# Kernel optimization log

Measured on AMD Instinct MI355X. Metric: run time of the kernel, lower is better.

## Reference

```python
import jax, jax.numpy as jnp
import numpy as np

D_MODEL = 192
NODE_NUM = 64
DEPTH = 2
ALPHA = 0.05
NUM_LAYERS = 2
LN_EPS = 1e-5


def _gcn(x, p):
    # x: [N, in_dim*D_MODEL]; faithful port of GCN.forward (eval mode)
    nv1, nv2, ws, bs, wm, bm, we, be, wl, bl, g, b = p
    N = x.shape[0]
    in_dim = x.shape[1] // D_MODEL
    adp = jax.nn.softmax(jax.nn.relu(nv1 @ nv2), axis=1)            # [V,V]
    adj = adp + jnp.eye(NODE_NUM, dtype=x.dtype)
    a = adj / adj.sum(1, keepdims=True)                              # row-normalized
    h0 = jax.lax.conv_general_dilated(
        x.reshape(N, in_dim, D_MODEL), ws, (1,), 'VALID',
        dimension_numbers=('NCH', 'OIH', 'NCH')) + bs[None, :, None]  # [N,C,V]
    h = h0
    outs = [h0]
    for _ in range(DEPTH):
        h = ALPHA * h0 + (1.0 - ALPHA) * jnp.einsum('ncw,vw->ncv', h, a)
        outs.append(h)
    ho = jnp.concatenate(outs, axis=1)                               # [N,(DEPTH+1)C,V]
    ho = jax.nn.gelu(jnp.einsum('ncv,oc->nov', ho, wm) + bm[None, :, None], approximate=False)
    ho = jnp.einsum('ncv,oc->nov', ho, we) + be[None, :, None]       # [N,6,V]
    ho = jnp.einsum('nov,dv->nod', ho, wl) + bl                      # [N,6,D]
    mu = ho.mean(-1, keepdims=True)
    var = ((ho - mu) ** 2).mean(-1, keepdims=True)                   # biased, like torch LN
    ho = (ho - mu) / jnp.sqrt(var + LN_EPS) * g + b
    return ho.reshape(N, 6 * D_MODEL)


def _encoder(inp4, flag, layer_params):
    x = jnp.transpose(inp4, (2, 0, 1, 3)) if flag == 1 else jnp.transpose(inp4, (1, 0, 2, 3))
    W, B, O, D = x.shape
    L = W + O - 1
    N = W * B
    # input_transfer: shift row r by r along the slice axis
    place = jax.vmap(lambda xr, r: jax.lax.dynamic_update_slice(
        jnp.zeros((B, L, D), x.dtype), xr, (0, r, 0)))
    a = place(x, jnp.arange(W)).reshape(N, L, D)
    layer0_output = None
    output_all = None
    rows_layers, cols_layers = [], []
    for layer in range(NUM_LAYERS):
        if layer >= 1:
            a = output_all  # eval mode: F.dropout is identity
            if layer == 1:
                layer0_output = a
        p = layer_params[layer]

        def step(carry, x_t, p=p):
            h_row, h_col = carry
            gate = _gcn(jnp.concatenate([h_row, h_col, x_t], axis=-1), p)  # [N,6D]
            sg = jax.nn.sigmoid(gate[:, :4 * D])
            tg = jnp.tanh(gate[:, 4 * D:])
            ug_r, og_r, ug_c, og_c = jnp.split(sg, 4, axis=-1)
            ig_r, ig_c = jnp.split(tg, 2, axis=-1)
            h_row = jnp.tanh((1.0 - ug_r) * h_row + ug_r * ig_r) * og_r
            h_col = jnp.tanh((1.0 - ug_c) * h_col + ug_c * ig_c) * og_c
            out_s = jnp.concatenate([h_row, h_col], axis=-1)
            # col hidden is saved pre-roll, rolled for next step
            return (h_row, jnp.roll(h_col, B, axis=0)), (out_s, h_row, h_col)

        init = (jnp.zeros((N, D), x.dtype), jnp.zeros((N, D), x.dtype))
        _, (outs, hrows, hcols) = jax.lax.scan(step, init, jnp.swapaxes(a, 0, 1))
        output_all = jnp.swapaxes(outs, 0, 1)                        # [N,L,2D]
        if layer >= 1:
            output_all = output_all + layer0_output
        # rows saved at slice s>=O-1 from block loc = s-O+1
        rows = hrows.reshape(L, W, B, D)[jnp.arange(O - 1, L), jnp.arange(W)]  # [W,B,D]
        # cols saved at slice s>=W-1 from last batch block
        cols = hcols[W - 1:, (W - 1) * B:, :]                        # [O,B,D]
        rows_layers.append(rows)
        cols_layers.append(cols)
    hidden_row_all = jnp.stack(rows_layers).transpose(2, 0, 1, 3)    # [B,layers,W,D]
    hidden_col_all = jnp.stack(cols_layers).transpose(2, 0, 1, 3)    # [B,layers,O,D]
    if flag == 1:
        return output_all, hidden_col_all, hidden_row_all
    return output_all, hidden_row_all, hidden_col_all


def setup_inputs() -> dict:
    key = jax.random.key(0)
    ks = jax.random.split(key, 20)
    idx = [0]
    def nxt():
        k = ks[idx[0]]
        idx[0] += 1
        return k
    B, W, O = 8, 24, 48
    K = D_MODEL - NODE_NUM + 1  # 129
    cc, sc, nd = 16, 32, 40
    d = {"input": jax.random.normal(nxt(), (B, W, O, D_MODEL), dtype=jnp.float32)}
    for li, in_dim in enumerate([3, 4]):
        d[f"nodevec1_{li}"] = jax.random.normal(nxt(), (NODE_NUM, nd), dtype=jnp.float32)
        d[f"nodevec2_{li}"] = jax.random.normal(nxt(), (nd, NODE_NUM), dtype=jnp.float32)
        d[f"w_start_{li}"] = jax.random.normal(nxt(), (cc, in_dim, K), dtype=jnp.float32) * 0.05
        d[f"b_start_{li}"] = jnp.zeros((cc,), jnp.float32)
        d[f"w_mlp_{li}"] = jax.random.normal(nxt(), (sc, (DEPTH + 1) * cc), dtype=jnp.float32) * 0.05
        d[f"b_mlp_{li}"] = jnp.zeros((sc,), jnp.float32)
        d[f"w_end_{li}"] = jax.random.normal(nxt(), (6, sc), dtype=jnp.float32) * 0.05
        d[f"b_end_{li}"] = jnp.zeros((6,), jnp.float32)
        d[f"w_lin_{li}"] = jax.random.normal(nxt(), (D_MODEL, NODE_NUM), dtype=jnp.float32) * 0.05
        d[f"b_lin_{li}"] = jnp.zeros((D_MODEL,), jnp.float32)
        d[f"gamma_{li}"] = jnp.ones((D_MODEL,), jnp.float32)
        d[f"beta_{li}"] = jnp.zeros((D_MODEL,), jnp.float32)
    d["flag"] = 0
    return d


def reference(input, nodevec1_0, nodevec2_0, w_start_0, b_start_0, w_mlp_0, b_mlp_0,
              w_end_0, b_end_0, w_lin_0, b_lin_0, gamma_0, beta_0,
              nodevec1_1, nodevec2_1, w_start_1, b_start_1, w_mlp_1, b_mlp_1,
              w_end_1, b_end_1, w_lin_1, b_lin_1, gamma_1, beta_1, flag):
    p0 = (nodevec1_0, nodevec2_0, w_start_0, b_start_0, w_mlp_0, b_mlp_0,
          w_end_0, b_end_0, w_lin_0, b_lin_0, gamma_0, beta_0)
    p1 = (nodevec1_1, nodevec2_1, w_start_1, b_start_1, w_mlp_1, b_mlp_1,
          w_end_1, b_end_1, w_lin_1, b_lin_1, gamma_1, beta_1)
    return _encoder(input, flag, (p0, p1))
```

## Files before the change

### kernel.cpp

```cpp
#include <hip/hip_runtime.h>
#include <hip/hip_bf16.h>

#define NT 512
typedef unsigned short u16;
typedef unsigned long long u64;

__device__ __forceinline__ u16 tobf(float x) {
  union { __hip_bfloat16 h; u16 u; } cv;
  cv.h = __float2bfloat16(x);
  return cv.u;
}
__device__ __forceinline__ float frombf(u16 u) {
  return __uint_as_float(((unsigned)u) << 16);
}
__device__ __forceinline__ float sigf(float x) {
  return __builtin_amdgcn_rcpf(1.f + __builtin_amdgcn_exp2f(-1.4426950408889634f * x));
}
__device__ __forceinline__ float tanh_fast(float x) {
  return 1.f - 2.f * __builtin_amdgcn_rcpf(1.f + __builtin_amdgcn_exp2f(2.8853900817779268f * x));
}
__device__ __forceinline__ void lds_fence() {
  asm volatile("s_waitcnt lgkmcnt(0)" ::: "memory");
  __builtin_amdgcn_sched_barrier(0);
}
__device__ __forceinline__ void bar_light() {
  asm volatile("s_waitcnt lgkmcnt(0)" ::: "memory");
  __builtin_amdgcn_s_barrier();
  asm volatile("" ::: "memory");
}

struct SeqArgs {
  const float* input;
  const float* nv1_0; const float* nv2_0; const float* nv1_1; const float* nv2_1;
  const float* w_start0; const float* b_start0; const float* w_mlp0; const float* b_mlp0;
  const float* w_end0;   const float* b_end0;   const float* w_lin0; const float* b_lin0;
  const float* gamma0;   const float* beta0;
  const float* w_start1; const float* b_start1; const float* w_mlp1; const float* b_mlp1;
  const float* w_end1;   const float* b_end1;   const float* w_lin1; const float* b_lin1;
  const float* gamma1;   const float* beta1;
  u64*   HCOL2;
  int*   prog;
  float* out_all; float* out_hrow; float* out_hcol;
};

__global__ __launch_bounds__(NT, 2) void seq_kernel(SeqArgs A) {
  const int n = blockIdx.x, w = n >> 3, b = n & 7, tid = threadIdx.x;
  const int pred = (n + 184) % 192;
  const int succ = (n + 8) % 192;

  __shared__ __align__(16) float sCIN[768];
  __shared__ __align__(16) u16   sWS[64 * 132];
  __shared__ __align__(16) float sAT[4096];
  __shared__ __align__(16) float sH[2][1024];
  __shared__ __align__(16) float sAbuf[4928];
  float* const sPart = sAbuf;
  float* const sG    = sAbuf;
  float* const sH2c  = sAbuf + 2048;
  float* const sE    = sAbuf + 2048;
  float* const sY    = sAbuf;
  float* const smWE  = sAbuf + 3072;
  float* const smBE  = sAbuf + 3264;
  float* const smWM  = sAbuf + 3328;

  for (int layer = 0; layer < 2; ++layer) {
    const int in_dim = 3 + layer;
    const int P = in_dim - 1;
    const float* nv1    = layer ? A.nv1_1    : A.nv1_0;
    const float* nv2    = layer ? A.nv2_1    : A.nv2_0;
    const float* wstart = layer ? A.w_start1 : A.w_start0;
    const float* bs     = layer ? A.b_start1 : A.b_start0;
    const float* wm     = layer ? A.w_mlp1   : A.w_mlp0;
    const float* bm     = layer ? A.b_mlp1   : A.b_mlp0;
    const float* we     = layer ? A.w_end1   : A.w_end0;
    const float* be     = layer ? A.b_end1   : A.b_end0;
    const float* wl     = layer ? A.w_lin1   : A.w_lin0;
    const float* bl     = layer ? A.b_lin1   : A.b_lin0;
    const float* gm     = layer ? A.gamma1   : A.gamma0;
    const float* bt     = layer ? A.beta1    : A.beta0;

    for (int idx = tid; idx < 4096; idx += NT) {
      int v = idx >> 6, ww = idx & 63;
      float s = 0.f;
      for (int j = 0; j < 40; ++j) s = fmaf(nv1[v*40 + j], nv2[j*64 + ww], s);
      sAbuf[idx] = fmaxf(s, 0.f);
    }
    __syncthreads();
    if (tid < 64) {
      const int v = tid;
      float m = -1e30f;
      for (int ww = 0; ww < 64; ++ww) m = fmaxf(m, sAbuf[v*64 + ww]);
      float s = 0.f;
      for (int ww = 0; ww < 64; ++ww) { float e = expf(sAbuf[v*64 + ww] - m); sAbuf[v*64 + ww] = e; s += e; }
      float inv = 1.f / s, rs = 1.f;
      for (int ww = 0; ww < 64; ++ww) rs += sAbuf[v*64 + ww] * inv;
      float irs = 1.f / rs;
      for (int ww = 0; ww < 64; ++ww) {
        float a = sAbuf[v*64 + ww] * inv + ((ww == v) ? 1.f : 0.f);
        sAT[ww*64 + v] = a * irs;
      }
    }
    __syncthreads();
    for (int idx = tid; idx < 16*in_dim*132; idx += NT) {
      int row = idx / 132, k = idx - row*132;
      sWS[idx] = (k < 129) ? tobf(wstart[((row & 15)*in_dim + (row >> 4))*129 + k]) : (u16)0;
    }
    for (int idx = tid; idx < 1536; idx += NT) { int o = idx/48, c = idx - o*48; smWM[o*50 + c] = wm[idx]; }
    for (int idx = tid; idx < 192; idx += NT) smWE[idx] = we[idx];
    if (tid < 6) smBE[tid] = be[tid];
    for (int d = tid; d < 384; d += NT) sCIN[d] = 0.f;

    const int v_p = tid & 63;
    const int o0  = tid >> 6;
    const float bmv0 = bm[o0], bmv1 = bm[o0 + 8], bmv2 = bm[o0 + 16], bmv3 = bm[o0 + 24];
    float blv = 0.f, gmv = 1.f, btv = 0.f;
    if (tid < 384) blv = bl[(tid >= 192) ? tid - 192 : tid];
    if (tid < 192) { gmv = gm[tid]; btv = bt[tid]; }
    float bs_r[2];
    bs_r[0] = bs[tid >> 6];
    bs_r[1] = bs[(tid >> 6) + 8];
    __syncthreads();

    auto pre_conv = [&]() {
      const int nslots = P << 8;
      for (int s = tid; s < nslots; s += NT) {
        const int cidx = s >> 4;
        const int p = cidx >> 4, c = cidx & 15;
        const int vg = s & 15;
        const int ich = (p == 0) ? 0 : (p + 1);
        const float* xin = ((p == 0) ? &sCIN[0] : &sCIN[384 + (p-1)*192]) + vg*4;
        const u16* wrow = &sWS[(ich*16 + c)*132];
        float a0 = 0.f, a1 = 0.f, a2 = 0.f, a3 = 0.f;
        float4 xc = *(const float4*)xin;
        for (int k4 = 0; k4 < 128; k4 += 4) {
          ushort4 wu = *(const ushort4*)(wrow + k4);
          float w0 = frombf(wu.x), w1 = frombf(wu.y), w2 = frombf(wu.z), w3 = frombf(wu.w);
          float4 xn = *(const float4*)(xin + k4 + 4);
          a0 = fmaf(w3, xc.w, fmaf(w2, xc.z, fmaf(w1, xc.y, fmaf(w0, xc.x, a0))));
          a1 = fmaf(w3, xn.x, fmaf(w2, xc.w, fmaf(w1, xc.z, fmaf(w0, xc.y, a1))));
          a2 = fmaf(w3, xn.y, fmaf(w2, xn.x, fmaf(w1, xc.w, fmaf(w0, xc.z, a2))));
          a3 = fmaf(w3, xn.z, fmaf(w2, xn.y, fmaf(w1, xn.x, fmaf(w0, xc.w, a3))));
          xc = xn;
        }
        float wk = frombf(wrow[128]);
        a0 = fmaf(wk, xc.x, a0); a1 = fmaf(wk, xc.y, a1);
        a2 = fmaf(wk, xc.z, a2); a3 = fmaf(wk, xc.w, a3);
        *(float4*)&sPart[cidx*64 + vg*4] = make_float4(a0, a1, a2, a3);
      }
      bar_light();
      {
        const int c0 = tid >> 6, v = tid & 63;
        float sum0 = bs_r[0], sum1 = bs_r[1];
        for (int p = 0; p < P; ++p) {
          sum0 += sPart[(p*16 + c0     )*64 + v];
          sum1 += sPart[(p*16 + c0 + 8 )*64 + v];
        }
        sH[0][ c0      *64 + v] = sum0;
        sH[0][(c0 + 8 )*64 + v] = sum1;
      }
      bar_light();
    };

    {
      if (layer == 0) {
        int o = 0 - w;
        if (o >= 0 && o < 48) {
          const float* xr = A.input + (((size_t)(b*24 + w)*48 + o)*192);
          for (int d = tid; d < 192; d += NT) sCIN[384 + d] = xr[d];
        } else {
          for (int d = tid; d < 192; d += NT) sCIN[384 + d] = 0.f;
        }
      } else {
        const float* xr = A.out_all + ((size_t)n*71 + 0)*384;
        for (int d = tid; d < 384; d += NT) sCIN[384 + d] = xr[d];
      }
      bar_light();
      pre_conv();
    }

    for (int t = 0; t < 71; ++t) {
      const int S = layer*71 + t;

      float xpa = 0.f, xpb = 0.f;
      if (t < 70 && tid < 192) {
        if (layer == 0) {
          int o = (t + 1) - w;
          if (o >= 0 && o < 48)
            xpa = A.input[(((size_t)(b*24 + w)*48 + o)*192) + tid];
        } else {
          const float* xr = A.out_all + ((size_t)n*71 + (t+1))*384;
          xpa = xr[tid];
          xpb = xr[192 + tid];
        }
      }

      if (t > 0) {
        if (tid < 192) {
          const u64* src = &A.HCOL2[((size_t)((S-1) & 15)*192 + pred)*192 + tid];
          u64 v;
          do {
            v = __hip_atomic_load(src, __ATOMIC_RELAXED, __HIP_MEMORY_SCOPE_AGENT);
          } while ((unsigned)(v >> 32) != (unsigned)S);
          sCIN[192 + tid] = __uint_as_float((unsigned)v);
        } else if (tid == 256 && S >= 16) {
          while (__hip_atomic_load(&A.prog[succ*32], __ATOMIC_RELAXED, __HIP_MEMORY_SCOPE_AGENT) < S - 15)
            __builtin_amdgcn_s_sleep(2);
        }
        bar_light();
        if (tid == 0)
          __hip_atomic_store(&A.prog[n*32], S, __ATOMIC_RELAXED, __HIP_MEMORY_SCOPE_AGENT);
      } else if (S >= 16) {
        if (tid == 256) {
          while (__hip_atomic_load(&A.prog[succ*32], __ATOMIC_RELAXED, __HIP_MEMORY_SCOPE_AGENT) < S - 15)
            __builtin_amdgcn_s_sleep(2);
        }
      }

      {
        const int c = tid >> 5, vg2 = tid & 31;
        const int vbase = c*64 + vg2*2;
        const float* xin = &sCIN[192 + vg2*2];
        const u16* wrow = &sWS[(16 + c)*132];
        float a0 = sH[0][vbase], a1 = sH[0][vbase + 1];
        float2 xc = *(const float2*)xin;
        for (int k2 = 0; k2 < 128; k2 += 2) {
          ushort2 wu = *(const ushort2*)(wrow + k2);
          float w0 = frombf(wu.x), w1 = frombf(wu.y);
          float2 xn = *(const float2*)(xin + k2 + 2);
          a0 = fmaf(w1, xc.y, fmaf(w0, xc.x, a0));
          a1 = fmaf(w1, xn.x, fmaf(w0, xc.y, a1));
          xc = xn;
        }
        float wk = frombf(wrow[128]);
        a0 = fmaf(wk, xc.x, a0); a1 = fmaf(wk, xc.y, a1);
        sH[0][vbase] = a0; sH[0][vbase + 1] = a1;
      }
      lds_fence();
      {
        const int c0 = o0 * 2;
        float pa0 = 0.f, pa1 = 0.f;
        for (int w4 = 0; w4 < 64; w4 += 4) {
          float a0v = sAT[(w4+0)*64 + v_p];
          float a1v = sAT[(w4+1)*64 + v_p];
          float a2v = sAT[(w4+2)*64 + v_p];
          float a3v = sAT[(w4+3)*64 + v_p];
          float4 h0v = *(const float4*)&sH[0][ c0      *64 + w4];
          float4 h1v = *(const float4*)&sH[0][(c0 + 1 )*64 + w4];
          pa0 = fmaf(h0v.x, a0v, pa0); pa0 = fmaf(h0v.y, a1v, pa0);
          pa0 = fmaf(h0v.z, a2v, pa0); pa0 = fmaf(h0v.w, a3v, pa0);
          pa1 = fmaf(h1v.x, a0v, pa1); pa1 = fmaf(h1v.y, a1v, pa1);
          pa1 = fmaf(h1v.z, a2v, pa1); pa1 = fmaf(h1v.w, a3v, pa1);
        }
        float h0a = sH[0][ c0      *64 + v_p];
        float h0b = sH[0][(c0 + 1 )*64 + v_p];
        sH[1][ c0      *64 + v_p] = fmaf(0.95f, pa0, 0.05f * h0a);
        sH[1][(c0 + 1 )*64 + v_p] = fmaf(0.95f, pa1, 0.05f * h0b);
        lds_fence();
        float pb0 = 0.f, pb1 = 0.f;
        for (int w4 = 0; w4 < 64; w4 += 4) {
          float a0v = sAT[(w4+0)*64 + v_p];
          float a1v = sAT[(w4+1)*64 + v_p];
          float a2v = sAT[(w4+2)*64 + v_p];
          float a3v = sAT[(w4+3)*64 + v_p];
          float4 h0v = *(const float4*)&sH[1][ c0      *64 + w4];
          float4 h1v = *(const float4*)&sH[1][(c0 + 1 )*64 + w4];
          pb0 = fmaf(h0v.x, a0v, pb0); pb0 = fmaf(h0v.y, a1v, pb0);
          pb0 = fmaf(h0v.z, a2v, pb0); pb0 = fmaf(h0v.w, a3v, pb0);
          pb1 = fmaf(h1v.x, a0v, pb1); pb1 = fmaf(h1v.y, a1v, pb1);
          pb1 = fmaf(h1v.z, a2v, pb1); pb1 = fmaf(h1v.w, a3v, pb1);
        }
        sH2c[ c0      *64 + v_p] = fmaf(0.95f, pb0, 0.05f * h0a);
        sH2c[(c0 + 1 )*64 + v_p] = fmaf(0.95f, pb1, 0.05f * h0b);
      }
      bar_light();

      {
        float g0 = bmv0, g1 = bmv1, g2 = bmv2, g3 = bmv3;
#pragma unroll
        for (int c = 0; c < 16; ++c) {
          float h0v = sH[0][c*64 + v_p];
          float h1v = sH[1][c*64 + v_p];
          float h2v = sH2c[c*64 + v_p];
          g0 = fmaf(smWM[(o0     )*50 + c], h0v, fmaf(smWM[(o0     )*50 + 16 + c], h1v, fmaf(smWM[(o0     )*50 + 32 + c], h2v, g0)));
          g1 = fmaf(smWM[(o0 +  8)*50 + c], h0v, fmaf(smWM[(o0 +  8)*50 + 16 + c], h1v, fmaf(smWM[(o0 +  8)*50 + 32 + c], h2v, g1)));
          g2 = fmaf(smWM[(o0 + 16)*50 + c], h0v, fmaf(smWM[(o0 + 16)*50 + 16 + c], h1v, fmaf(smWM[(o0 + 16)*50 + 32 + c], h2v, g2)));
          g3 = fmaf(smWM[(o0 + 24)*50 + c], h0v, fmaf(smWM[(o0 + 24)*50 + 16 + c], h1v, fmaf(smWM[(o0 + 24)*50 + 32 + c], h2v, g3)));
        }
        g0 = 0.5f * g0 * (1.f + erff(g0 * 0.70710678118654752f));
        g1 = 0.5f * g1 * (1.f + erff(g1 * 0.70710678118654752f));
        g2 = 0.5f * g2 * (1.f + erff(g2 * 0.70710678118654752f));
        g3 = 0.5f * g3 * (1.f + erff(g3 * 0.70710678118654752f));
        sG[(o0     )*64 + v_p] = g0;
        sG[(o0 +  8)*64 + v_p] = g1;
        sG[(o0 + 16)*64 + v_p] = g2;
        sG[(o0 + 24)*64 + v_p] = g3;
      }
      bar_light();

      for (int idx = tid; idx < 384; idx += NT) {
        int o2 = idx >> 6, v = idx & 63;
        float acc = smBE[o2];
        for (int c = 0; c < 32; ++c) acc = fmaf(smWE[o2*32 + c], sG[c*64 + v], acc);
        sE[idx] = acc;
      }
      bar_light();

      if (tid < 384) {
        const int d  = (tid >= 192) ? tid - 192 : tid;
        const int r0 = (tid >= 192) ? 3 : 0;
        const float4* wrow = (const float4*)(wl + d*64);
        float y0 = blv, y1 = blv, y2 = blv;
        for (int q = 0; q < 16; ++q) {
          float4 wv = wrow[q];
          float4 e0 = *(const float4*)&sE[(r0+0)*64 + q*4];
          float4 e1 = *(const float4*)&sE[(r0+1)*64 + q*4];
          float4 e2 = *(const float4*)&sE[(r0+2)*64 + q*4];
          y0 = fmaf(e0.x,wv.x, fmaf(e0.y,wv.y, fmaf(e0.z,wv.z, fmaf(e0.w,wv.w, y0))));
          y1 = fmaf(e1.x,wv.x, fmaf(e1.y,wv.y, fmaf(e1.z,wv.z, fmaf(e1.w,wv.w, y1))));
          y2 = fmaf(e2.x,wv.x, fmaf(e2.y,wv.y, fmaf(e2.z,wv.z, fmaf(e2.w,wv.w, y2))));
        }
        sY[(r0+0)*192 + d] = y0;
        sY[(r0+1)*192 + d] = y1;
        sY[(r0+2)*192 + d] = y2;
      }
      bar_light();

      if (tid < 192) {
        const int r = tid >> 5, l32 = tid & 31;
        float sm = 0.f, sq = 0.f;
#pragma unroll
        for (int m = 0; m < 6; ++m) {
          float v = sY[r*192 + l32 + 32*m];
          sm += v; sq = fmaf(v, v, sq);
        }
#pragma unroll
        for (int off = 16; off >= 1; off >>= 1) {
          sm += __shfl_xor(sm, off);
          sq += __shfl_xor(sq, off);
        }
        if (l32 == 0) {
          float mu = sm * (1.f/192.f);
          float var = sq * (1.f/192.f) - mu*mu;
          sH[1][r] = mu;
          sH[1][8 + r] = rsqrtf(fmaxf(var, 0.f) + 1e-5f);
        }
      }
      bar_light();

      float hcn = 0.f;
      if (tid < 192) {
        const int d = tid;
        float y2 = fmaf((sY[2*192+d] - sH[1][2]) * sH[1][10], gmv, btv);
        float y3 = fmaf((sY[3*192+d] - sH[1][3]) * sH[1][11], gmv, btv);
        float y5 = fmaf((sY[5*192+d] - sH[1][5]) * sH[1][13], gmv, btv);
        float ugc = sigf(y2), ogc = sigf(y3), igc = tanh_fast(y5);
        float hc = sCIN[192 + d];
        hcn = tanh_fast(fmaf(ugc, igc, (1.f - ugc)*hc)) * ogc;
        u64 pk = ((u64)(unsigned)(S + 1) << 32) | (u64)__float_as_uint(hcn);
        __hip_atomic_store(&A.HCOL2[((size_t)(S & 15)*192 + n)*192 + d], pk,
                           __ATOMIC_RELAXED, __HIP_MEMORY_SCOPE_AGENT);
      }
      if (tid < 192) {
        const int d = tid;
        float y0 = fmaf((sY[0*192+d] - sH[1][0]) * sH[1][8],  gmv, btv);
        float y1 = fmaf((sY[1*192+d] - sH[1][1]) * sH[1][9],  gmv, btv);
        float y4 = fmaf((sY[4*192+d] - sH[1][4]) * sH[1][12], gmv, btv);
        float ugr = sigf(y0), ogr = sigf(y1), igr = tanh_fast(y4);
        float hr = sCIN[d];
        float hrn = tanh_fast(fmaf(ugr, igr, (1.f - ugr)*hr)) * ogr;
        sCIN[d] = hrn;
        float* oa = A.out_all + ((size_t)n*71 + t)*384;
        if (layer == 0) { oa[d] = hrn; oa[192 + d] = hcn; }
        else           { oa[d] = hrn + sCIN[384 + d]; oa[192 + d] = hcn + sCIN[576 + d]; }
        if (t == 47 + w)
          A.out_hrow[(((size_t)b*2 + layer)*24 + w)*192 + d] = hrn;
        if (w == 23 && t >= 23)
          A.out_hcol[(((size_t)b*2 + layer)*48 + (t - 23))*192 + d] = hcn;
        if (t < 70) {
          sCIN[384 + d] = xpa;
          if (layer == 1) sCIN[576 + d] = xpb;
        }
      }
      bar_light();
      if (t < 70) pre_conv();
    }
    __syncthreads();
  }
}

extern "C" void kernel_launch(void* const* d_in, const int* in_sizes, int n_in,
                              void* d_out, int out_size, void* d_ws, size_t ws_size,
                              hipStream_t stream) {
  (void)in_sizes; (void)n_in; (void)out_size; (void)ws_size;
  char* ws = (char*)d_ws;
  int* prog  = (int*)ws;
  u64* HCOL2 = (u64*)(ws + 24576);

  hipMemsetAsync(ws, 0, 24576 + 4718592, stream);

  SeqArgs A;
  A.input    = (const float*)d_in[0];
  A.nv1_0    = (const float*)d_in[1];  A.nv2_0 = (const float*)d_in[2];
  A.w_start0 = (const float*)d_in[3];  A.b_start0 = (const float*)d_in[4];
  A.w_mlp0   = (const float*)d_in[5];  A.b_mlp0   = (const float*)d_in[6];
  A.w_end0   = (const float*)d_in[7];  A.b_end0   = (const float*)d_in[8];
  A.w_lin0   = (const float*)d_in[9];  A.b_lin0   = (const float*)d_in[10];
  A.gamma0   = (const float*)d_in[11]; A.beta0    = (const float*)d_in[12];
  A.nv1_1    = (const float*)d_in[13]; A.nv2_1 = (const float*)d_in[14];
  A.w_start1 = (const float*)d_in[15]; A.b_start1 = (const float*)d_in[16];
  A.w_mlp1   = (const float*)d_in[17]; A.b_mlp1   = (const float*)d_in[18];
  A.w_end1   = (const float*)d_in[19]; A.b_end1   = (const float*)d_in[20];
  A.w_lin1   = (const float*)d_in[21]; A.b_lin1   = (const float*)d_in[22];
  A.gamma1   = (const float*)d_in[23]; A.beta1    = (const float*)d_in[24];
  A.HCOL2 = HCOL2; A.prog = prog;
  A.out_all  = (float*)d_out;
  A.out_hrow = (float*)d_out + 5234688;
  A.out_hcol = (float*)d_out + 5308416;

  seq_kernel<<<192, NT, 0, stream>>>(A);
}
```

Before: 2.644 ms.

## Double block size, split next-input prefetch to spare waves, double-buffer inputs

The block grows to 1024 threads. The first 512 threads run the recurrent conv and graph propagation. The other 512 prefetch the next step's input directly into a double-buffered LDS slot and poll the successor's progress flag. Work in pre_conv and the MLP stage is repartitioned so each thread handles fewer outputs, and the hcol spin-wait now sleeps between polls. This aims to hide global-load latency and shorten per-step critical-path work, at the cost of more waves per block and fewer idle lanes in some phases.

```diff
diff --git a/kernel.cpp b/kernel.cpp
--- a/kernel.cpp
+++ b/kernel.cpp
@@ -1,7 +1,7 @@
 #include <hip/hip_runtime.h>
 #include <hip/hip_bf16.h>
 
-#define NT 512
+#define NT 1024
 typedef unsigned short u16;
 typedef unsigned long long u64;
 
@@ -43,12 +43,12 @@
   float* out_all; float* out_hrow; float* out_hcol;
 };
 
-__global__ __launch_bounds__(NT, 2) void seq_kernel(SeqArgs A) {
+__global__ __launch_bounds__(NT, 4) void seq_kernel(SeqArgs A) {
   const int n = blockIdx.x, w = n >> 3, b = n & 7, tid = threadIdx.x;
   const int pred = (n + 184) % 192;
   const int succ = (n + 8) % 192;
 
-  __shared__ __align__(16) float sCIN[768];
+  __shared__ __align__(16) float sCIN[1152];
   __shared__ __align__(16) u16   sWS[64 * 132];
   __shared__ __align__(16) float sAT[4096];
   __shared__ __align__(16) float sH[2][1024];
@@ -111,116 +111,24 @@
 
     const int v_p = tid & 63;
     const int o0  = tid >> 6;
-    const float bmv0 = bm[o0], bmv1 = bm[o0 + 8], bmv2 = bm[o0 + 16], bmv3 = bm[o0 + 24];
+    const float bmv0 = bm[o0], bmv1 = bm[o0 + 16];
     float blv = 0.f, gmv = 1.f, btv = 0.f;
     if (tid < 384) blv = bl[(tid >= 192) ? tid - 192 : tid];
     if (tid < 192) { gmv = gm[tid]; btv = bt[tid]; }
-    float bs_r[2];
-    bs_r[0] = bs[tid >> 6];
-    bs_r[1] = bs[(tid >> 6) + 8];
+    const float bs_r0 = bs[o0];
     __syncthreads();
 
-    auto pre_conv = [&]() {
-      const int nslots = P << 8;
+    auto pre_conv = [&](int parity) {
+      const float* xb = &sCIN[384 + parity*384];
+      const int nslots = P << 9;
       for (int s = tid; s < nslots; s += NT) {
-        const int cidx = s >> 4;
+        const int cidx = s >> 5;
+        const int vg2  = s & 31;
         const int p = cidx >> 4, c = cidx & 15;
-        const int vg = s & 15;
         const int ich = (p == 0) ? 0 : (p + 1);
-        const float* xin = ((p == 0) ? &sCIN[0] : &sCIN[384 + (p-1)*192]) + vg*4;
+        const float* xin = ((p == 0) ? &sCIN[0] : &xb[(p-1)*192]) + vg2*2;
         const u16* wrow = &sWS[(ich*16 + c)*132];
-        float a0 = 0.f, a1 = 0.f, a2 = 0.f, a3 = 0.f;
-        float4 xc = *(const float4*)xin;
-        for (int k4 = 0; k4 < 128; k4 += 4) {
-          ushort4 wu = *(const ushort4*)(wrow + k4);
-          float w0 = frombf(wu.x), w1 = frombf(wu.y), w2 = frombf(wu.z), w3 = frombf(wu.w);
-          float4 xn = *(const float4*)(xin + k4 + 4);
-          a0 = fmaf(w3, xc.w, fmaf(w2, xc.z, fmaf(w1, xc.y, fmaf(w0, xc.x, a0))));
-          a1 = fmaf(w3, xn.x, fmaf(w2, xc.w, fmaf(w1, xc.z, fmaf(w0, xc.y, a1))));
-          a2 = fmaf(w3, xn.y, fmaf(w2, xn.x, fmaf(w1, xc.w, fmaf(w0, xc.z, a2))));
-          a3 = fmaf(w3, xn.z, fmaf(w2, xn.y, fmaf(w1, xn.x, fmaf(w0, xc.w, a3))));
-          xc = xn;
-        }
-        float wk = frombf(wrow[128]);
-        a0 = fmaf(wk, xc.x, a0); a1 = fmaf(wk, xc.y, a1);
-        a2 = fmaf(wk, xc.z, a2); a3 = fmaf(wk, xc.w, a3);
-        *(float4*)&sPart[cidx*64 + vg*4] = make_float4(a0, a1, a2, a3);
-      }
-      bar_light();
-      {
-        const int c0 = tid >> 6, v = tid & 63;
-        float sum0 = bs_r[0], sum1 = bs_r[1];
-        for (int p = 0; p < P; ++p) {
-          sum0 += sPart[(p*16 + c0     )*64 + v];
-          sum1 += sPart[(p*16 + c0 + 8 )*64 + v];
-        }
-        sH[0][ c0      *64 + v] = sum0;
-        sH[0][(c0 + 8 )*64 + v] = sum1;
-      }
-      bar_light();
-    };
-
-    {
-      if (layer == 0) {
-        int o = 0 - w;
-        if (o >= 0 && o < 48) {
-          const float* xr = A.input + (((size_t)(b*24 + w)*48 + o)*192);
-          for (int d = tid; d < 192; d += NT) sCIN[384 + d] = xr[d];
-        } else {
-          for (int d = tid; d < 192; d += NT) sCIN[384 + d] = 0.f;
-        }
-      } else {
-        const float* xr = A.out_all + ((size_t)n*71 + 0)*384;
-        for (int d = tid; d < 384; d += NT) sCIN[384 + d] = xr[d];
-      }
-      bar_light();
-      pre_conv();
-    }
-
-    for (int t = 0; t < 71; ++t) {
-      const int S = layer*71 + t;
-
-      float xpa = 0.f, xpb = 0.f;
-      if (t < 70 && tid < 192) {
-        if (layer == 0) {
-          int o = (t + 1) - w;
-          if (o >= 0 && o < 48)
-            xpa = A.input[(((size_t)(b*24 + w)*48 + o)*192) + tid];
-        } else {
-          const float* xr = A.out_all + ((size_t)n*71 + (t+1))*384;
-          xpa = xr[tid];
-          xpb = xr[192 + tid];
-        }
-      }
-
-      if (t > 0) {
-        if (tid < 192) {
-          const u64* src = &A.HCOL2[((size_t)((S-1) & 15)*192 + pred)*192 + tid];
-          u64 v;
-          do {
-            v = __hip_atomic_load(src, __ATOMIC_RELAXED, __HIP_MEMORY_SCOPE_AGENT);
-          } while ((unsigned)(v >> 32) != (unsigned)S);
-          sCIN[192 + tid] = __uint_as_float((unsigned)v);
-        } else if (tid == 256 && S >= 16) {
-          while (__hip_atomic_load(&A.prog[succ*32], __ATOMIC_RELAXED, __HIP_MEMORY_SCOPE_AGENT) < S - 15)
-            __builtin_amdgcn_s_sleep(2);
-        }
-        bar_light();
-        if (tid == 0)
-          __hip_atomic_store(&A.prog[n*32], S, __ATOMIC_RELAXED, __HIP_MEMORY_SCOPE_AGENT);
-      } else if (S >= 16) {
-        if (tid == 256) {
-          while (__hip_atomic_load(&A.prog[succ*32], __ATOMIC_RELAXED, __HIP_MEMORY_SCOPE_AGENT) < S - 15)
-            __builtin_amdgcn_s_sleep(2);
-        }
-      }
-
-      {
-        const int c = tid >> 5, vg2 = tid & 31;
-        const int vbase = c*64 + vg2*2;
-        const float* xin = &sCIN[192 + vg2*2];
-        const u16* wrow = &sWS[(16 + c)*132];
-        float a0 = sH[0][vbase], a1 = sH[0][vbase + 1];
+        float a0 = 0.f, a1 = 0.f;
         float2 xc = *(const float2*)xin;
         for (int k2 = 0; k2 < 128; k2 += 2) {
           ushort2 wu = *(const ushort2*)(wrow + k2);
@@ -232,67 +140,148 @@
         }
         float wk = frombf(wrow[128]);
         a0 = fmaf(wk, xc.x, a0); a1 = fmaf(wk, xc.y, a1);
-        sH[0][vbase] = a0; sH[0][vbase + 1] = a1;
-      }
-      lds_fence();
+        *(float2*)&sPart[cidx*64 + vg2*2] = make_float2(a0, a1);
+      }
+      bar_light();
       {
-        const int c0 = o0 * 2;
-        float pa0 = 0.f, pa1 = 0.f;
-        for (int w4 = 0; w4 < 64; w4 += 4) {
-          float a0v = sAT[(w4+0)*64 + v_p];
-          float a1v = sAT[(w4+1)*64 + v_p];
-          float a2v = sAT[(w4+2)*64 + v_p];
-          float a3v = sAT[(w4+3)*64 + v_p];
-          float4 h0v = *(const float4*)&sH[0][ c0      *64 + w4];
-          float4 h1v = *(const float4*)&sH[0][(c0 + 1 )*64 + w4];
-          pa0 = fmaf(h0v.x, a0v, pa0); pa0 = fmaf(h0v.y, a1v, pa0);
-          pa0 = fmaf(h0v.z, a2v, pa0); pa0 = fmaf(h0v.w, a3v, pa0);
-          pa1 = fmaf(h1v.x, a0v, pa1); pa1 = fmaf(h1v.y, a1v, pa1);
-          pa1 = fmaf(h1v.z, a2v, pa1); pa1 = fmaf(h1v.w, a3v, pa1);
-        }
-        float h0a = sH[0][ c0      *64 + v_p];
-        float h0b = sH[0][(c0 + 1 )*64 + v_p];
-        sH[1][ c0      *64 + v_p] = fmaf(0.95f, pa0, 0.05f * h0a);
-        sH[1][(c0 + 1 )*64 + v_p] = fmaf(0.95f, pa1, 0.05f * h0b);
+        const int c0 = o0, v = v_p;
+        float sum = bs_r0;
+        for (int p = 0; p < P; ++p) sum += sPart[(p*16 + c0)*64 + v];
+        sH[0][c0*64 + v] = sum;
+      }
+      bar_light();
+    };
+
+    {
+      float* xb = &sCIN[384];
+      if (layer == 0) {
+        int o = 0 - w;
+        if (o >= 0 && o < 48) {
+          const float* xr = A.input + (((size_t)(b*24 + w)*48 + o)*192);
+          for (int d = tid; d < 192; d += NT) xb[d] = xr[d];
+        } else {
+          for (int d = tid; d < 192; d += NT) xb[d] = 0.f;
+        }
+      } else {
+        const float* xr = A.out_all + ((size_t)n*71 + 0)*384;
+        for (int d = tid; d < 384; d += NT) xb[d] = xr[d];
+      }
+      bar_light();
+      pre_conv(0);
+    }
+
+    for (int t = 0; t < 71; ++t) {
+      const int S = layer*71 + t;
+
+      if (t > 0) {
+        if (tid < 192) {
+          const u64* src = &A.HCOL2[((size_t)((S-1) & 15)*192 + pred)*192 + tid];
+          u64 v = __hip_atomic_load(src, __ATOMIC_RELAXED, __HIP_MEMORY_SCOPE_AGENT);
+          while ((unsigned)(v >> 32) != (unsigned)S) {
+            __builtin_amdgcn_s_sleep(1);
+            v = __hip_atomic_load(src, __ATOMIC_RELAXED, __HIP_MEMORY_SCOPE_AGENT);
+          }
+          __builtin_amdgcn_sched_barrier(0);
+          asm volatile("" ::: "memory");
+          sCIN[192 + tid] = __uint_as_float((unsigned)v);
+        }
+        bar_light();
+        if (tid == 0)
+          __hip_atomic_store(&A.prog[n*32], S, __ATOMIC_RELAXED, __HIP_MEMORY_SCOPE_AGENT);
+      }
+
+      if (tid < 512) {
+        {
+          const int c = tid >> 5, vg2 = tid & 31;
+          const int vbase = c*64 + vg2*2;
+          const float* xin = &sCIN[192 + vg2*2];
+          const u16* wrow = &sWS[(16 + c)*132];
+          float a0 = sH[0][vbase], a1 = sH[0][vbase + 1];
+          float2 xc = *(const float2*)xin;
+          for (int k2 = 0; k2 < 128; k2 += 2) {
+            ushort2 wu = *(const ushort2*)(wrow + k2);
+            float w0 = frombf(wu.x), w1 = frombf(wu.y);
+            float2 xn = *(const float2*)(xin + k2 + 2);
+            a0 = fmaf(w1, xc.y, fmaf(w0, xc.x, a0));
+            a1 = fmaf(w1, xn.x, fmaf(w0, xc.y, a1));
+            xc = xn;
+          }
+          float wk = frombf(wrow[128]);
+          a0 = fmaf(wk, xc.x, a0); a1 = fmaf(wk, xc.y, a1);
+          sH[0][vbase] = a0; sH[0][vbase + 1] = a1;
+        }
         lds_fence();
-        float pb0 = 0.f, pb1 = 0.f;
-        for (int w4 = 0; w4 < 64; w4 += 4) {
-          float a0v = sAT[(w4+0)*64 + v_p];
-          float a1v = sAT[(w4+1)*64 + v_p];
-          float a2v = sAT[(w4+2)*64 + v_p];
-          float a3v = sAT[(w4+3)*64 + v_p];
-          float4 h0v = *(const float4*)&sH[1][ c0      *64 + w4];
-          float4 h1v = *(const float4*)&sH[1][(c0 + 1 )*64 + w4];
-          pb0 = fmaf(h0v.x, a0v, pb0); pb0 = fmaf(h0v.y, a1v, pb0);
-          pb0 = fmaf(h0v.z, a2v, pb0); pb0 = fmaf(h0v.w, a3v, pb0);
-          pb1 = fmaf(h1v.x, a0v, pb1); pb1 = fmaf(h1v.y, a1v, pb1);
-          pb1 = fmaf(h1v.z, a2v, pb1); pb1 = fmaf(h1v.w, a3v, pb1);
-        }
-        sH2c[ c0      *64 + v_p] = fmaf(0.95f, pb0, 0.05f * h0a);
-        sH2c[(c0 + 1 )*64 + v_p] = fmaf(0.95f, pb1, 0.05f * h0b);
+        {
+          const int c0 = o0 * 2;
+          float pa0 = 0.f, pa1 = 0.f;
+          for (int w4 = 0; w4 < 64; w4 += 4) {
+            float a0v = sAT[(w4+0)*64 + v_p];
+            float a1v = sAT[(w4+1)*64 + v_p];
+            float a2v = sAT[(w4+2)*64 + v_p];
+            float a3v = sAT[(w4+3)*64 + v_p];
+            float4 h0v = *(const float4*)&sH[0][ c0      *64 + w4];
+            float4 h1v = *(const float4*)&sH[0][(c0 + 1 )*64 + w4];
+            pa0 = fmaf(h0v.x, a0v, pa0); pa0 = fmaf(h0v.y, a1v, pa0);
+            pa0 = fmaf(h0v.z, a2v, pa0); pa0 = fmaf(h0v.w, a3v, pa0);
+            pa1 = fmaf(h1v.x, a0v, pa1); pa1 = fmaf(h1v.y, a1v, pa1);
+            pa1 = fmaf(h1v.z, a2v, pa1); pa1 = fmaf(h1v.w, a3v, pa1);
+          }
+          float h0a = sH[0][ c0      *64 + v_p];
+          float h0b = sH[0][(c0 + 1 )*64 + v_p];
+          sH[1][ c0      *64 + v_p] = fmaf(0.95f, pa0, 0.05f * h0a);
+          sH[1][(c0 + 1 )*64 + v_p] = fmaf(0.95f, pa1, 0.05f * h0b);
+          lds_fence();
+          float pb0 = 0.f, pb1 = 0.f;
+          for (int w4 = 0; w4 < 64; w4 += 4) {
+            float a0v = sAT[(w4+0)*64 + v_p];
+            float a1v = sAT[(w4+1)*64 + v_p];
+            float a2v = sAT[(w4+2)*64 + v_p];
+            float a3v = sAT[(w4+3)*64 + v_p];
+            float4 h0v = *(const float4*)&sH[1][ c0      *64 + w4];
+            float4 h1v = *(const float4*)&sH[1][(c0 + 1 )*64 + w4];
+            pb0 = fmaf(h0v.x, a0v, pb0); pb0 = fmaf(h0v.y, a1v, pb0);
+            pb0 = fmaf(h0v.z, a2v, pb0); pb0 = fmaf(h0v.w, a3v, pb0);
+            pb1 = fmaf(h1v.x, a0v, pb1); pb1 = fmaf(h1v.y, a1v, pb1);
+            pb1 = fmaf(h1v.z, a2v, pb1); pb1 = fmaf(h1v.w, a3v, pb1);
+          }
+          sH2c[ c0      *64 + v_p] = fmaf(0.95f, pb0, 0.05f * h0a);
+          sH2c[(c0 + 1 )*64 + v_p] = fmaf(0.95f, pb1, 0.05f * h0b);
+        }
+      } else {
+        if (t < 70) {
+          const int d = tid - 512;
+          float* xb = &sCIN[384 + ((t+1) & 1)*384];
+          if (layer == 0) {
+            if (d < 192) {
+              int o = (t + 1) - w;
+              xb[d] = (o >= 0 && o < 48)
+                    ? A.input[(((size_t)(b*24 + w)*48 + o)*192) + d] : 0.f;
+            }
+          } else {
+            if (d < 384) xb[d] = A.out_all[((size_t)n*71 + (t+1))*384 + d];
+          }
+        }
+        if (tid == 960 && S >= 16) {
+          while (__hip_atomic_load(&A.prog[succ*32], __ATOMIC_RELAXED, __HIP_MEMORY_SCOPE_AGENT) < S - 15)
+            __builtin_amdgcn_s_sleep(2);
+        }
       }
       bar_light();
 
       {
-        float g0 = bmv0, g1 = bmv1, g2 = bmv2, g3 = bmv3;
+        float g0 = bmv0, g1 = bmv1;
 #pragma unroll
         for (int c = 0; c < 16; ++c) {
           float h0v = sH[0][c*64 + v_p];
           float h1v = sH[1][c*64 + v_p];
           float h2v = sH2c[c*64 + v_p];
-          g0 = fmaf(smWM[(o0     )*50 + c], h0v, fmaf(smWM[(o0     )*50 + 16 + c], h1v, fmaf(smWM[(o0     )*50 + 32 + c], h2v, g0)));
-          g1 = fmaf(smWM[(o0 +  8)*50 + c], h0v, fmaf(smWM[(o0 +  8)*50 + 16 + c], h1v, fmaf(smWM[(o0 +  8)*50 + 32 + c], h2v, g1)));
-          g2 = fmaf(smWM[(o0 + 16)*50 + c], h0v, fmaf(smWM[(o0 + 16)*50 + 16 + c], h1v, fmaf(smWM[(o0 + 16)*50 + 32 + c], h2v, g2)));
-          g3 = fmaf(smWM[(o0 + 24)*50 + c], h0v, fmaf(smWM[(o0 + 24)*50 + 16 + c], h1v, fmaf(smWM[(o0 + 24)*50 + 32 + c], h2v, g3)));
+          g0 = fmaf(smWM[ o0      *50 + c], h0v, fmaf(smWM[ o0      *50 + 16 + c], h1v, fmaf(smWM[ o0      *50 + 32 + c], h2v, g0)));
+          g1 = fmaf(smWM[(o0+16 )*50 + c], h0v, fmaf(smWM[(o0+16 )*50 + 16 + c], h1v, fmaf(smWM[(o0+16 )*50 + 32 + c], h2v, g1)));
         }
         g0 = 0.5f * g0 * (1.f + erff(g0 * 0.70710678118654752f));
         g1 = 0.5f * g1 * (1.f + erff(g1 * 0.70710678118654752f));
-        g2 = 0.5f * g2 * (1.f + erff(g2 * 0.70710678118654752f));
-        g3 = 0.5f * g3 * (1.f + erff(g3 * 0.70710678118654752f));
-        sG[(o0     )*64 + v_p] = g0;
-        sG[(o0 +  8)*64 + v_p] = g1;
-        sG[(o0 + 16)*64 + v_p] = g2;
-        sG[(o0 + 24)*64 + v_p] = g3;
+        sG[ o0      *64 + v_p] = g0;
+        sG[(o0+16 )*64 + v_p] = g1;
       }
       bar_light();
 
@@ -370,18 +359,17 @@
         sCIN[d] = hrn;
         float* oa = A.out_all + ((size_t)n*71 + t)*384;
         if (layer == 0) { oa[d] = hrn; oa[192 + d] = hcn; }
-        else           { oa[d] = hrn + sCIN[384 + d]; oa[192 + d] = hcn + sCIN[576 + d]; }
+        else {
+          const float* xbt = &sCIN[384 + (t & 1)*384];
+          oa[d] = hrn + xbt[d]; oa[192 + d] = hcn + xbt[192 + d];
+        }
         if (t == 47 + w)
           A.out_hrow[(((size_t)b*2 + layer)*24 + w)*192 + d] = hrn;
         if (w == 23 && t >= 23)
           A.out_hcol[(((size_t)b*2 + layer)*48 + (t - 23))*192 + d] = hcn;
-        if (t < 70) {
-          sCIN[384 + d] = xpa;
-          if (layer == 1) sCIN[576 + d] = xpb;
-        }
-      }
-      bar_light();
-      if (t < 70) pre_conv();
+      }
+      bar_light();
+      if (t < 70) pre_conv((t + 1) & 1);
     }
     __syncthreads();
   }
```

New measurement: 2.674 ms. Within noise of the previous version (+1.1%).

## Prefetch predecessor hcol during gate phase and store conv weights as fp32

Applied to the files above, without the earlier changes.

A spare wavefront (threads 448-511) now polls the predecessor block's packed HCOL2 entries for the next step during the current step's gate computation. It writes them into a double-buffered LDS array and sets a flag so the next step can skip its blocking spin wait. The start-conv weights are also kept in LDS as fp32 (rounded through bf16 to keep the same values) instead of bf16, which removes the per-element conversions. This doubles that LDS footprint and adds bounded polling work plus a flag handshake whose ordering must be correct.

```diff
diff --git a/kernel.cpp b/kernel.cpp
--- a/kernel.cpp
+++ b/kernel.cpp
@@ -49,10 +49,12 @@
   const int succ = (n + 8) % 192;
 
   __shared__ __align__(16) float sCIN[768];
-  __shared__ __align__(16) u16   sWS[64 * 132];
+  __shared__ __align__(16) float sWSf[64 * 132];
   __shared__ __align__(16) float sAT[4096];
   __shared__ __align__(16) float sH[2][1024];
   __shared__ __align__(16) float sAbuf[4928];
+  __shared__ __align__(16) float sHCbuf[2][192];
+  __shared__ int sPreOK;
   float* const sPart = sAbuf;
   float* const sG    = sAbuf;
   float* const sH2c  = sAbuf + 2048;
@@ -102,12 +104,14 @@
     __syncthreads();
     for (int idx = tid; idx < 16*in_dim*132; idx += NT) {
       int row = idx / 132, k = idx - row*132;
-      sWS[idx] = (k < 129) ? tobf(wstart[((row & 15)*in_dim + (row >> 4))*129 + k]) : (u16)0;
+      sWSf[idx] = (k < 129) ? frombf(tobf(wstart[((row & 15)*in_dim + (row >> 4))*129 + k])) : 0.f;
     }
     for (int idx = tid; idx < 1536; idx += NT) { int o = idx/48, c = idx - o*48; smWM[o*50 + c] = wm[idx]; }
     for (int idx = tid; idx < 192; idx += NT) smWE[idx] = we[idx];
     if (tid < 6) smBE[tid] = be[tid];
-    for (int d = tid; d < 384; d += NT) sCIN[d] = 0.f;
+    for (int d = tid; d < 192; d += NT) sCIN[d] = 0.f;
+    for (int d = tid; d < 384; d += NT) ((float*)sHCbuf)[d] = 0.f;
+    if (tid == 0) sPreOK = 0;
 
     const int v_p = tid & 63;
     const int o0  = tid >> 6;
@@ -128,20 +132,19 @@
         const int vg = s & 15;
         const int ich = (p == 0) ? 0 : (p + 1);
         const float* xin = ((p == 0) ? &sCIN[0] : &sCIN[384 + (p-1)*192]) + vg*4;
-        const u16* wrow = &sWS[(ich*16 + c)*132];
+        const float* wrow = &sWSf[(ich*16 + c)*132];
         float a0 = 0.f, a1 = 0.f, a2 = 0.f, a3 = 0.f;
         float4 xc = *(const float4*)xin;
         for (int k4 = 0; k4 < 128; k4 += 4) {
-          ushort4 wu = *(const ushort4*)(wrow + k4);
-          float w0 = frombf(wu.x), w1 = frombf(wu.y), w2 = frombf(wu.z), w3 = frombf(wu.w);
+          float4 wv = *(const float4*)(wrow + k4);
           float4 xn = *(const float4*)(xin + k4 + 4);
-          a0 = fmaf(w3, xc.w, fmaf(w2, xc.z, fmaf(w1, xc.y, fmaf(w0, xc.x, a0))));
-          a1 = fmaf(w3, xn.x, fmaf(w2, xc.w, fmaf(w1, xc.z, fmaf(w0, xc.y, a1))));
-          a2 = fmaf(w3, xn.y, fmaf(w2, xn.x, fmaf(w1, xc.w, fmaf(w0, xc.z, a2))));
-          a3 = fmaf(w3, xn.z, fmaf(w2, xn.y, fmaf(w1, xn.x, fmaf(w0, xc.w, a3))));
+          a0 = fmaf(wv.w, xc.w, fmaf(wv.z, xc.z, fmaf(wv.y, xc.y, fmaf(wv.x, xc.x, a0))));
+          a1 = fmaf(wv.w, xn.x, fmaf(wv.z, xc.w, fmaf(wv.y, xc.z, fmaf(wv.x, xc.y, a1))));
+          a2 = fmaf(wv.w, xn.y, fmaf(wv.z, xn.x, fmaf(wv.y, xc.w, fmaf(wv.x, xc.z, a2))));
+          a3 = fmaf(wv.w, xn.z, fmaf(wv.z, xn.y, fmaf(wv.y, xn.x, fmaf(wv.x, xc.w, a3))));
           xc = xn;
         }
-        float wk = frombf(wrow[128]);
+        float wk = wrow[128];
         a0 = fmaf(wk, xc.x, a0); a1 = fmaf(wk, xc.y, a1);
         a2 = fmaf(wk, xc.z, a2); a3 = fmaf(wk, xc.w, a3);
         *(float4*)&sPart[cidx*64 + vg*4] = make_float4(a0, a1, a2, a3);
@@ -194,43 +197,51 @@
       }
 
       if (t > 0) {
+        const int pok = sPreOK;
         if (tid < 192) {
-          const u64* src = &A.HCOL2[((size_t)((S-1) & 15)*192 + pred)*192 + tid];
-          u64 v;
-          do {
-            v = __hip_atomic_load(src, __ATOMIC_RELAXED, __HIP_MEMORY_SCOPE_AGENT);
-          } while ((unsigned)(v >> 32) != (unsigned)S);
-          sCIN[192 + tid] = __uint_as_float((unsigned)v);
+          if (!pok) {
+            const u64* src = &A.HCOL2[((size_t)((S-1) & 15)*192 + pred)*192 + tid];
+            u64 v = __hip_atomic_load(src, __ATOMIC_RELAXED, __HIP_MEMORY_SCOPE_AGENT);
+            while ((unsigned)(v >> 32) != (unsigned)S) {
+              __builtin_amdgcn_s_sleep(1);
+              v = __hip_atomic_load(src, __ATOMIC_RELAXED, __HIP_MEMORY_SCOPE_AGENT);
+            }
+            __builtin_amdgcn_sched_barrier(0);
+            asm volatile("" ::: "memory");
+            sHCbuf[t & 1][tid] = __uint_as_float((unsigned)v);
+          }
         } else if (tid == 256 && S >= 16) {
           while (__hip_atomic_load(&A.prog[succ*32], __ATOMIC_RELAXED, __HIP_MEMORY_SCOPE_AGENT) < S - 15)
             __builtin_amdgcn_s_sleep(2);
         }
         bar_light();
-        if (tid == 0)
+        if (tid == 0) {
+          sPreOK = 0;
           __hip_atomic_store(&A.prog[n*32], S, __ATOMIC_RELAXED, __HIP_MEMORY_SCOPE_AGENT);
+        }
       } else if (S >= 16) {
         if (tid == 256) {
           while (__hip_atomic_load(&A.prog[succ*32], __ATOMIC_RELAXED, __HIP_MEMORY_SCOPE_AGENT) < S - 15)
             __builtin_amdgcn_s_sleep(2);
         }
+        if (tid == 0) sPreOK = 0;
       }
 
       {
         const int c = tid >> 5, vg2 = tid & 31;
         const int vbase = c*64 + vg2*2;
-        const float* xin = &sCIN[192 + vg2*2];
-        const u16* wrow = &sWS[(16 + c)*132];
+        const float* xin = &sHCbuf[t & 1][vg2*2];
+        const float* wrow = &sWSf[(16 + c)*132];
         float a0 = sH[0][vbase], a1 = sH[0][vbase + 1];
         float2 xc = *(const float2*)xin;
         for (int k2 = 0; k2 < 128; k2 += 2) {
-          ushort2 wu = *(const ushort2*)(wrow + k2);
-          float w0 = frombf(wu.x), w1 = frombf(wu.y);
+          float2 wv = *(const float2*)(wrow + k2);
           float2 xn = *(const float2*)(xin + k2 + 2);
-          a0 = fmaf(w1, xc.y, fmaf(w0, xc.x, a0));
-          a1 = fmaf(w1, xn.x, fmaf(w0, xc.y, a1));
+          a0 = fmaf(wv.y, xc.y, fmaf(wv.x, xc.x, a0));
+          a1 = fmaf(wv.y, xn.x, fmaf(wv.x, xc.y, a1));
           xc = xn;
         }
-        float wk = frombf(wrow[128]);
+        float wk = wrow[128];
         a0 = fmaf(wk, xc.x, a0); a1 = fmaf(wk, xc.y, a1);
         sH[0][vbase] = a0; sH[0][vbase + 1] = a1;
       }
@@ -353,11 +364,50 @@
         float y3 = fmaf((sY[3*192+d] - sH[1][3]) * sH[1][11], gmv, btv);
         float y5 = fmaf((sY[5*192+d] - sH[1][5]) * sH[1][13], gmv, btv);
         float ugc = sigf(y2), ogc = sigf(y3), igc = tanh_fast(y5);
-        float hc = sCIN[192 + d];
+        float hc = sHCbuf[t & 1][d];
         hcn = tanh_fast(fmaf(ugc, igc, (1.f - ugc)*hc)) * ogc;
         u64 pk = ((u64)(unsigned)(S + 1) << 32) | (u64)__float_as_uint(hcn);
         __hip_atomic_store(&A.HCOL2[((size_t)(S & 15)*192 + n)*192 + d], pk,
                            __ATOMIC_RELAXED, __HIP_MEMORY_SCOPE_AGENT);
+      } else if (tid >= 448 && t < 70) {
+        const int l = tid - 448;
+        const unsigned Sn = (unsigned)(S + 1);
+        const u64* base = &A.HCOL2[((size_t)(S & 15)*192 + pred)*192];
+        bool ok = true;
+        u64 v0, v1, v2;
+        {
+          const u64* src = base + l;
+          v0 = __hip_atomic_load(src, __ATOMIC_RELAXED, __HIP_MEMORY_SCOPE_AGENT);
+          for (int sp = 0; sp < 16 && (unsigned)(v0 >> 32) != Sn; ++sp) {
+            __builtin_amdgcn_s_sleep(1);
+            v0 = __hip_atomic_load(src, __ATOMIC_RELAXED, __HIP_MEMORY_SCOPE_AGENT);
+          }
+          ok &= ((unsigned)(v0 >> 32) == Sn);
+        }
+        {
+          const u64* src = base + l + 64;
+          v1 = __hip_atomic_load(src, __ATOMIC_RELAXED, __HIP_MEMORY_SCOPE_AGENT);
+          for (int sp = 0; sp < 16 && (unsigned)(v1 >> 32) != Sn; ++sp) {
+            __builtin_amdgcn_s_sleep(1);
+            v1 = __hip_atomic_load(src, __ATOMIC_RELAXED, __HIP_MEMORY_SCOPE_AGENT);
+          }
+          ok &= ((unsigned)(v1 >> 32) == Sn);
+        }
+        {
+          const u64* src = base + l + 128;
+          v2 = __hip_atomic_load(src, __ATOMIC_RELAXED, __HIP_MEMORY_SCOPE_AGENT);
+          for (int sp = 0; sp < 16 && (unsigned)(v2 >> 32) != Sn; ++sp) {
+            __builtin_amdgcn_s_sleep(1);
+            v2 = __hip_atomic_load(src, __ATOMIC_RELAXED, __HIP_MEMORY_SCOPE_AGENT);
+          }
+          ok &= ((unsigned)(v2 >> 32) == Sn);
+        }
+        float* dstb = &sHCbuf[(t + 1) & 1][0];
+        dstb[l]       = __uint_as_float((unsigned)v0);
+        dstb[l + 64]  = __uint_as_float((unsigned)v1);
+        dstb[l + 128] = __uint_as_float((unsigned)v2);
+        u64 bal = __ballot(ok);
+        if (l == 0) sPreOK = (bal == ~0ull) ? 1 : 0;
       }
       if (tid < 192) {
         const int d = tid;
@@ -395,7 +445,7 @@
   int* prog  = (int*)ws;
   u64* HCOL2 = (u64*)(ws + 24576);
 
-  hipMemsetAsync(ws, 0, 24576 + 4718592, stream);
+  (void)hipMemsetAsync(ws, 0, 24576 + 4718592, stream);
 
   SeqArgs A;
   A.input    = (const float*)d_in[0];
```

Result: slower. 2.715 ms (+2.7%).
